# Optimization experiments

Hardware: AMD Instinct MI355X
Metric: run time of the kernel (lower is better)

Reference implementation:

```python
import jax, jax.numpy as jnp
import numpy as np

B, S, D_IN, D_OUT, H = 4, 2048, 1024, 1024, 16
HD = D_OUT // H  # 64


def setup_inputs() -> dict:
    key = jax.random.key(0)
    ks = jax.random.split(key, 6)
    s = 1.0 / np.sqrt(D_IN)
    return {
        "x": jax.random.normal(ks[0], (B, S, D_IN), dtype=jnp.float32),
        "Wq": jax.random.uniform(ks[1], (D_IN, D_OUT), jnp.float32, -s, s),
        "Wk": jax.random.uniform(ks[2], (D_IN, D_OUT), jnp.float32, -s, s),
        "Wv": jax.random.uniform(ks[3], (D_IN, D_OUT), jnp.float32, -s, s),
        "Wo": jax.random.uniform(ks[4], (D_OUT, D_OUT), jnp.float32, -s, s),
        "bo": jax.random.uniform(ks[5], (D_OUT,), jnp.float32, -s, s),
    }


def reference(x, Wq, Wk, Wv, Wo, bo):
    b, s, _ = x.shape
    # QKV projections -> [b, H, s, hd]
    def split_heads(t):
        return t.reshape(b, s, H, HD).transpose(0, 2, 1, 3)
    q = split_heads(x @ Wq)
    k = split_heads(x @ Wk)
    v = split_heads(x @ Wv)
    # attention scores [b, H, s, s]
    scores = jnp.einsum("bhqd,bhkd->bhqk", q, k)
    causal = jnp.triu(jnp.ones((s, s), dtype=bool), k=1)
    scores = jnp.where(causal, -jnp.inf, scores)
    attn = jax.nn.softmax(scores / np.sqrt(HD), axis=-1)
    ctx = jnp.einsum("bhqk,bhkd->bhqd", attn, v)
    ctx = ctx.transpose(0, 2, 1, 3).reshape(b, s, D_OUT)
    return ctx @ Wo + bo
```

## Files before the change

kernel.cpp:

```cpp
#include <hip/hip_runtime.h>

typedef __attribute__((ext_vector_type(8))) short bf16x8;
typedef __attribute__((ext_vector_type(4))) float f32x4;
typedef __attribute__((ext_vector_type(4))) unsigned uint4v;

#define SM_C 0.18033688011112042f
#define MFMA16 __builtin_amdgcn_mfma_f32_16x16x32_bf16

__device__ __forceinline__ unsigned short f2bf(float f) {
  unsigned u = __builtin_bit_cast(unsigned, f);
  u += 0x7fffu + ((u >> 16) & 1u);
  return (unsigned short)(u >> 16);
}

__device__ __forceinline__ unsigned cvtpk(float lo, float hi) {
  unsigned r;
  asm volatile("v_cvt_pk_bf16_f32 %0, %1, %2" : "=v"(r) : "v"(lo), "v"(hi));
  return r;
}

__device__ __forceinline__ void gload16(const void* g, void* lds) {
  __builtin_amdgcn_global_load_lds(
      (const __attribute__((address_space(1))) void*)g,
      (__attribute__((address_space(3))) void*)lds, 16, 0, 0);
}

#define BARRIER __builtin_amdgcn_s_barrier()
#define LGKM0 asm volatile("s_waitcnt lgkmcnt(0)" ::: "memory")

__global__ __launch_bounds__(256) void cvt_x(const float* __restrict__ in,
                                             unsigned short* __restrict__ out,
                                             int n4) {
  int i = blockIdx.x * 256 + threadIdx.x;
  int stride = gridDim.x * 256;
  for (; i < n4; i += stride) {
    float4 v = ((const float4*)in)[i];
    unsigned short o0 = f2bf(v.x), o1 = f2bf(v.y), o2 = f2bf(v.z), o3 = f2bf(v.w);
    unsigned long long packed = (unsigned long long)o0 | ((unsigned long long)o1 << 16) |
                                ((unsigned long long)o2 << 32) | ((unsigned long long)o3 << 48);
    ((unsigned long long*)out)[i] = packed;
  }
}

__global__ __launch_bounds__(256) void transpose_w4(const float* __restrict__ W0,
                                                    const float* __restrict__ W1,
                                                    const float* __restrict__ W2,
                                                    const float* __restrict__ W3,
                                                    unsigned short* __restrict__ WT) {
  __shared__ float tile[32][33];
  const int z = blockIdx.z;
  const float* W = (z == 0) ? W0 : (z == 1) ? W1 : (z == 2) ? W2 : W3;
  unsigned short* WTo = WT + (size_t)z * 1048576;
  int bx = blockIdx.x, by = blockIdx.y;
  int x = bx * 32 + threadIdx.x;
  for (int i = 0; i < 4; ++i) {
    int r = threadIdx.y + i * 8;
    tile[r][threadIdx.x] = W[(by * 32 + r) * 1024 + x];
  }
  __syncthreads();
  int nx = by * 32 + threadIdx.x;
  for (int i = 0; i < 4; ++i) {
    int r = threadIdx.y + i * 8;
    WTo[(long)(bx * 32 + r) * 1024 + nx] = f2bf(tile[threadIdx.x][r]);
  }
}

__global__ __launch_bounds__(256) void transpose_v(const unsigned short* __restrict__ QKV,
                                                   unsigned short* __restrict__ Vt) {
  __shared__ alignas(16) unsigned short tile[64][74];
  const int bid = blockIdx.x;
  const int st = bid & 31, bh = bid >> 5;
  const int b = bh >> 4, h = bh & 15;
  const int t = threadIdx.x;
  const int r = t >> 2, c16 = (t & 3) * 16;
  const unsigned short* src =
      QKV + ((long)(b * 2048 + st * 64 + r)) * 3072 + 2048 + h * 64 + c16;
  uint4v v0 = *(const uint4v*)src;
  uint4v v1 = *(const uint4v*)(src + 8);
  unsigned* dst32 = (unsigned*)&tile[r][c16];
  dst32[0] = v0[0]; dst32[1] = v0[1]; dst32[2] = v0[2]; dst32[3] = v0[3];
  dst32[4] = v1[0]; dst32[5] = v1[1]; dst32[6] = v1[2]; dst32[7] = v1[3];
  __syncthreads();
  const int lw = t & 63, w = t >> 6;
  const int vp = (lw & 32) | (((lw >> 2) & 3) << 3) | (((lw >> 4) & 1) << 2) | (lw & 3);
#pragma unroll
  for (int k = 0; k < 16; ++k) {
    int hd = w * 16 + k;
    Vt[((long)(bh * 64 + hd)) * 2048 + st * 64 + vp] = tile[lw][hd];
  }
}

template <int NR, int FP32OUT>
__global__ __launch_bounds__(512, 1) void gemm2ph(const unsigned short* __restrict__ A,
                                                  const unsigned short* __restrict__ BT,
                                                  unsigned short* __restrict__ Cb,
                                                  float* __restrict__ Cf,
                                                  const float* __restrict__ bias,
                                                  int M, int N, int K) {
  constexpr int BN = NR * 64;
  __shared__ alignas(16) unsigned short As[2][256 * 64];
  __shared__ alignas(16) unsigned short Bs[2][BN * 64];

  const int nbn = N / BN;
  const int tmg = (M / 256) / 8;
  const int cc = blockIdx.x >> 3, xc = blockIdx.x & 7;
  const int tm = xc * tmg + cc / nbn, tn = cc % nbn;

  const int t = threadIdx.x, l = t & 63, wid = t >> 6;
  const int wm = wid >> 2, wn = wid & 3;
  const int lr = l & 15, lg = l >> 4;

  f32x4 acc[8][NR] = {};

  const int sq = t >> 3;
  const int sslot8 = ((t & 7) ^ (sq & 7)) * 8;
  const unsigned short* Ath = A + ((long)tm * 256 + sq) * K + sslot8;
  const unsigned short* Bth = BT + ((long)tn * BN + sq) * K + sslot8;
  const int ldsoff = sq * 64 + (t & 7) * 8;

#define STGA(buf, q, kt) \
  gload16(Ath + (long)((q)*64) * K + (kt)*64, &As[buf][(q)*4096 + ldsoff])
#define STGB(buf, u, kt) \
  gload16(Bth + (long)((u)*64) * K + (kt)*64, &Bs[buf][(u)*4096 + ldsoff])

  const int NT = K >> 6;
#pragma unroll
  for (int u = 0; u < NR; ++u) STGB(0, u, 0);
  STGA(0, 0, 0); STGA(0, 2, 0); STGA(0, 1, 0); STGA(0, 3, 0);

  const int offk0 = (lg ^ (lr & 7)) * 8;
  const int offk1 = ((4 + lg) ^ (lr & 7)) * 8;
  const int arow0 = (wm * 128 + lr) * 64;
  const int brow0 = (wn * (NR * 16) + lr) * 64;

#define DS_A(MH)                                                   \
  _Pragma("unroll") for (int m_ = 0; m_ < 4; ++m_) {               \
    const unsigned short* ap_ = Ac + arow0 + ((MH)*4 + m_) * 1024; \
    af[m_][0] = *(const bf16x8*)(ap_ + offk0);                     \
    af[m_][1] = *(const bf16x8*)(ap_ + offk1);                     \
  }
#define DS_B_ALL                                          \
  _Pragma("unroll") for (int n_ = 0; n_ < NR; ++n_) {     \
    const unsigned short* bp_ = Bc + brow0 + n_ * 1024;   \
    bfr[n_][0] = *(const bf16x8*)(bp_ + offk0);           \
    bfr[n_][1] = *(const bf16x8*)(bp_ + offk1);           \
  }
#define MM(MH)                                                              \
  __builtin_amdgcn_s_setprio(1);                                            \
  _Pragma("unroll") for (int m_ = 0; m_ < 4; ++m_)                          \
  _Pragma("unroll") for (int n_ = 0; n_ < NR; ++n_) {                       \
    acc[(MH)*4 + m_][n_] = MFMA16(af[m_][0], bfr[n_][0],                    \
                                  acc[(MH)*4 + m_][n_], 0, 0, 0);           \
    acc[(MH)*4 + m_][n_] = MFMA16(af[m_][1], bfr[n_][1],                    \
                                  acc[(MH)*4 + m_][n_], 0, 0, 0);           \
  }                                                                         \
  __builtin_amdgcn_s_setprio(0);

  for (int tt = 0; tt < NT; ++tt) {
    const unsigned short* Ac = As[tt & 1];
    const unsigned short* Bc = Bs[tt & 1];
    const int nb = (tt & 1) ^ 1;
    const int kt = tt + 1;
    const bool st = kt < NT;

    bf16x8 af[4][2];
    bf16x8 bfr[NR][2];

    asm volatile("s_waitcnt vmcnt(2)" ::: "memory");
    BARRIER;
    DS_A(0);
    DS_B_ALL;
    if (st) {
#pragma unroll
      for (int u = 0; u < NR; ++u) STGB(nb, u, kt);
    }
    BARRIER;
    LGKM0;
    MM(0);

    if (st) {
      if constexpr (NR == 3) asm volatile("s_waitcnt vmcnt(3)" ::: "memory");
      else                   asm volatile("s_waitcnt vmcnt(2)" ::: "memory");
    } else {
      asm volatile("s_waitcnt vmcnt(0)" ::: "memory");
    }
    BARRIER;
    DS_A(1);
    if (st) { STGA(nb, 0, kt); STGA(nb, 2, kt); STGA(nb, 1, kt); STGA(nb, 3, kt); }
    BARRIER;
    LGKM0;
    MM(1);
  }
#undef DS_A
#undef DS_B_ALL
#undef MM
#undef STGA
#undef STGB

  const long crow = (long)tm * 256 + wm * 128;
  const int ccol = tn * BN + wn * (NR * 16);
#pragma unroll
  for (int m = 0; m < 8; ++m)
#pragma unroll
    for (int n = 0; n < NR; ++n)
#pragma unroll
      for (int r = 0; r < 4; ++r) {
        long row = crow + m * 16 + lg * 4 + r;
        int col = ccol + n * 16 + lr;
        if (FP32OUT)
          Cf[row * N + col] = acc[m][n][r] + bias[col];
        else
          Cb[row * N + col] = f2bf(acc[m][n][r]);
      }
}

template <int TWO>
__device__ __forceinline__ void attn_tile(
    const unsigned short* __restrict__ Kc, const unsigned short* __restrict__ Vc,
    int lr, int lg, bool mask0, bool mask1, int kv0, int q0row, int q1row,
    const bf16x8 (&qf)[2][2], f32x4 (&cacc)[2][4], float (&m_r)[2], float (&l_r)[2]) {
  constexpr int S0 = TWO ? 0 : 1;
  f32x4 p[2][4];
#pragma unroll
  for (int s = S0; s < 2; ++s)
#pragma unroll
    for (int g = 0; g < 4; ++g) p[s][g] = f32x4{0.f, 0.f, 0.f, 0.f};

  __builtin_amdgcn_s_setprio(1);
#pragma unroll
  for (int g = 0; g < 4; ++g) {
    const int key = g * 16 + lr;
    const int swz = (key & 7) << 3;
#pragma unroll
    for (int c = 0; c < 2; ++c) {
      bf16x8 kf = *(const bf16x8*)(Kc + key * 64 + ((c * 32 + lg * 8) ^ swz));
#pragma unroll
      for (int s = S0; s < 2; ++s)
        p[s][g] = MFMA16(kf, qf[s][c], p[s][g], 0, 0, 0);
    }
  }
  __builtin_amdgcn_s_setprio(0);

  if (TWO && mask0) {
#pragma unroll
    for (int g = 0; g < 4; ++g)
#pragma unroll
      for (int r = 0; r < 4; ++r)
        if (kv0 + g * 16 + lg * 4 + r > q0row) p[0][g][r] = -1e30f;
  }
  if (mask1) {
#pragma unroll
    for (int g = 0; g < 4; ++g)
#pragma unroll
      for (int r = 0; r < 4; ++r)
        if (kv0 + g * 16 + lg * 4 + r > q1row) p[1][g][r] = -1e30f;
  }

  unsigned pk[2][4][2];
#pragma unroll
  for (int s = S0; s < 2; ++s) {
    float mloc = p[s][0][0];
#pragma unroll
    for (int g = 0; g < 4; ++g)
#pragma unroll
      for (int r = 0; r < 4; ++r) mloc = fmaxf(mloc, p[s][g][r]);
    mloc = fmaxf(mloc, __shfl_xor(mloc, 16));
    mloc = fmaxf(mloc, __shfl_xor(mloc, 32));
    const bool defer = __all(mloc <= m_r[s] + 44.0f);
    const float mn = defer ? m_r[s] : fmaxf(m_r[s], mloc);
    const float nmc = -mn * SM_C;
    float rs = 0.f;
#pragma unroll
    for (int g = 0; g < 4; ++g)
#pragma unroll
      for (int r = 0; r < 4; ++r) {
        float e = __builtin_amdgcn_exp2f(__builtin_fmaf(p[s][g][r], SM_C, nmc));
        p[s][g][r] = e;
        rs += e;
      }
    rs += __shfl_xor(rs, 16);
    rs += __shfl_xor(rs, 32);
    if (defer) {
      l_r[s] += rs;
    } else {
      float alpha = __builtin_amdgcn_exp2f((m_r[s] - mn) * SM_C);
      l_r[s] = l_r[s] * alpha + rs;
      m_r[s] = mn;
      float alq[4];
#pragma unroll
      for (int r = 0; r < 4; ++r) alq[r] = __shfl(alpha, lg * 20 + r);
#pragma unroll
      for (int n = 0; n < 4; ++n)
#pragma unroll
        for (int r = 0; r < 4; ++r) cacc[s][n][r] *= alq[r];
    }
#pragma unroll
    for (int g = 0; g < 4; ++g) {
      pk[s][g][0] = cvtpk(p[s][g][0], p[s][g][1]);
      pk[s][g][1] = cvtpk(p[s][g][2], p[s][g][3]);
    }
  }

#pragma unroll
  for (int sl = 0; sl < 2; ++sl) {
    bf16x8 vf[4];
#pragma unroll
    for (int n = 0; n < 4; ++n) {
      const int hd = n * 16 + lr;
      vf[n] = *(const bf16x8*)(Vc + hd * 64 + ((sl * 32 + lg * 8) ^ ((hd & 7) << 3)));
    }
    __builtin_amdgcn_s_setprio(1);
#pragma unroll
    for (int s = S0; s < 2; ++s) {
      uint4v pw = {pk[s][2 * sl][0], pk[s][2 * sl][1], pk[s][2 * sl + 1][0], pk[s][2 * sl + 1][1]};
      bf16x8 pa = __builtin_bit_cast(bf16x8, pw);
#pragma unroll
      for (int n = 0; n < 4; ++n)
        cacc[s][n] = MFMA16(pa, vf[n], cacc[s][n], 0, 0, 0);
    }
    __builtin_amdgcn_s_setprio(0);
  }
}

__global__ __launch_bounds__(256, 4) void flash_attn(const unsigned short* __restrict__ QKV,
                                                     const unsigned short* __restrict__ Vt,
                                                     unsigned short* __restrict__ Ctx) {
  __shared__ alignas(16) unsigned short Ks[2][64 * 64];
  __shared__ alignas(16) unsigned short Vs[2][64 * 64];
  const int bid = blockIdx.x;
  const int qt = bid >> 6;
  const int bh = bid & 63;
  const int b = bh >> 4, h = bh & 15;
  const int t = threadIdx.x, l = t & 63, w = t >> 6;
  const int lr = l & 15, lg = l >> 4;
  const long rowbase = (long)b * 2048;
  const int colbase = h * 64;
  const int q0 = qt * 64 + w * 16;
  const int q1 = (31 - qt) * 64 + w * 16;
  const int q0row = q0 + lr, q1row = q1 + lr;
  const int nkv = 32 - qt;

  bf16x8 qf[2][2];
#pragma unroll
  for (int c = 0; c < 2; ++c) {
    qf[0][c] = *(const bf16x8*)(QKV + (rowbase + q0 + lr) * 3072 + colbase + c * 32 + lg * 8);
    qf[1][c] = *(const bf16x8*)(QKV + (rowbase + q1 + lr) * 3072 + colbase + c * 32 + lg * 8);
  }

  f32x4 cacc[2][4];
  float m_r[2], l_r[2];
#pragma unroll
  for (int s = 0; s < 2; ++s) {
    m_r[s] = -1e30f;
    l_r[s] = 0.f;
#pragma unroll
    for (int n = 0; n < 4; ++n) cacc[s][n] = f32x4{0.f, 0.f, 0.f, 0.f};
  }

  const int srow = w * 16 + (l >> 3);
  const int scol = (l & 7) * 8;
  const int kswz = scol ^ ((srow & 7) << 3);
  const unsigned short* kp = QKV + (rowbase + srow) * 3072 + 1024 + colbase + kswz;
  const unsigned short* vp = Vt + ((long)(bh * 64 + srow)) * 2048 + kswz;
  unsigned short* ksd0 = &Ks[0][(w * 16) * 64];
  unsigned short* vsd0 = &Vs[0][(w * 16) * 64];

#define STAGE(buf)                                    \
  do {                                                \
    gload16(kp, ksd0 + (buf) * 4096);                 \
    gload16(kp + 8 * 3072, ksd0 + (buf) * 4096 + 512);\
    gload16(vp, vsd0 + (buf) * 4096);                 \
    gload16(vp + 8 * 2048, vsd0 + (buf) * 4096 + 512);\
    kp += 64 * 3072;                                  \
    vp += 64;                                         \
  } while (0)

  STAGE(0);
  __syncthreads();

  int j = 0;
  for (; j <= qt; ++j) {
    const int cur = j & 1;
    if (j + 1 < nkv) STAGE(cur ^ 1);
    attn_tile<1>(Ks[cur], Vs[cur], lr, lg, j == qt, false, j * 64, q0row, q1row,
                 qf, cacc, m_r, l_r);
    __syncthreads();
  }
  for (; j < nkv; ++j) {
    const int cur = j & 1;
    if (j + 1 < nkv) STAGE(cur ^ 1);
    attn_tile<0>(Ks[cur], Vs[cur], lr, lg, false, j == nkv - 1, j * 64, q0row, q1row,
                 qf, cacc, m_r, l_r);
    __syncthreads();
  }
#undef STAGE

#pragma unroll
  for (int s = 0; s < 2; ++s) {
    float invl = 1.f / l_r[s];
    float ilq[4];
#pragma unroll
    for (int r = 0; r < 4; ++r) ilq[r] = __shfl(invl, lg * 20 + r);
    const int qs = (s == 0) ? q0 : q1;
#pragma unroll
    for (int n = 0; n < 4; ++n)
#pragma unroll
      for (int r = 0; r < 4; ++r) {
        long row = rowbase + qs + lg * 4 + r;
        Ctx[row * 1024 + colbase + n * 16 + lr] = f2bf(cacc[s][n][r] * ilq[r]);
      }
  }
}

extern "C" void kernel_launch(void* const* d_in, const int* in_sizes, int n_in,
                              void* d_out, int out_size, void* d_ws, size_t ws_size,
                              hipStream_t stream) {
  (void)in_sizes; (void)n_in; (void)out_size; (void)ws_size;
  const float* x  = (const float*)d_in[0];
  const float* Wq = (const float*)d_in[1];
  const float* Wk = (const float*)d_in[2];
  const float* Wv = (const float*)d_in[3];
  const float* Wo = (const float*)d_in[4];
  const float* bo = (const float*)d_in[5];
  float* out = (float*)d_out;

  unsigned short* ws = (unsigned short*)d_ws;
  unsigned short* xb  = ws;
  unsigned short* Vt  = ws;
  unsigned short* WqT = ws + 8388608;
  unsigned short* WkT = WqT + 1048576;
  unsigned short* WvT = WkT + 1048576;
  unsigned short* WoT = WvT + 1048576;
  unsigned short* QKV = WoT + 1048576;
  unsigned short* Ctx = QKV + 25165824;

  cvt_x<<<2048, 256, 0, stream>>>(x, xb, 8192 * 1024 / 4);

  dim3 tb(32, 8), tg(32, 32, 4);
  transpose_w4<<<tg, tb, 0, stream>>>(Wq, Wk, Wv, Wo, WqT);

  gemm2ph<3, 0><<<512, 512, 0, stream>>>(xb, WqT, QKV, nullptr, nullptr,
                                         8192, 3072, 1024);

  transpose_v<<<2048, 256, 0, stream>>>(QKV, Vt);

  flash_attn<<<1024, 256, 0, stream>>>(QKV, Vt, Ctx);

  gemm2ph<2, 1><<<256, 512, 0, stream>>>(Ctx, WoT, nullptr, out, bo,
                                         8192, 1024, 1024);
}
```

Before: 160.2 us.

## Triple-buffer A tiles in GEMM to prefetch two K-steps ahead

The GEMM kernel now keeps three LDS buffers for the A operand instead of two. A tiles are prefetched two K-steps ahead while B stays double-buffered. This removes the mid-iteration waitcnt and barrier and gives global loads more time in flight. In exchange LDS use rises to about 144KB per block and the vmcnt bookkeeping becomes more delicate.

```diff
diff --git a/kernel.cpp b/kernel.cpp
--- a/kernel.cpp
+++ b/kernel.cpp
@@ -91,14 +91,14 @@
 }
 
 template <int NR, int FP32OUT>
-__global__ __launch_bounds__(512, 1) void gemm2ph(const unsigned short* __restrict__ A,
-                                                  const unsigned short* __restrict__ BT,
-                                                  unsigned short* __restrict__ Cb,
-                                                  float* __restrict__ Cf,
-                                                  const float* __restrict__ bias,
-                                                  int M, int N, int K) {
+__global__ __launch_bounds__(512, 1) void gemm3b(const unsigned short* __restrict__ A,
+                                                 const unsigned short* __restrict__ BT,
+                                                 unsigned short* __restrict__ Cb,
+                                                 float* __restrict__ Cf,
+                                                 const float* __restrict__ bias,
+                                                 int M, int N, int K) {
   constexpr int BN = NR * 64;
-  __shared__ alignas(16) unsigned short As[2][256 * 64];
+  __shared__ alignas(16) unsigned short As[3][256 * 64];
   __shared__ alignas(16) unsigned short Bs[2][BN * 64];
 
   const int nbn = N / BN;
@@ -125,8 +125,11 @@
 
   const int NT = K >> 6;
 #pragma unroll
+  for (int q = 0; q < 4; ++q) STGA(0, q, 0);
+#pragma unroll
   for (int u = 0; u < NR; ++u) STGB(0, u, 0);
-  STGA(0, 0, 0); STGA(0, 2, 0); STGA(0, 1, 0); STGA(0, 3, 0);
+#pragma unroll
+  for (int q = 0; q < 4; ++q) STGA(1, q, 1);
 
   const int offk0 = (lg ^ (lr & 7)) * 8;
   const int offk1 = ((4 + lg) ^ (lr & 7)) * 8;
@@ -156,40 +159,40 @@
   }                                                                         \
   __builtin_amdgcn_s_setprio(0);
 
+  int cur3 = 0;
+  int stg3 = 2;
   for (int tt = 0; tt < NT; ++tt) {
-    const unsigned short* Ac = As[tt & 1];
+    const unsigned short* Ac = As[cur3];
     const unsigned short* Bc = Bs[tt & 1];
-    const int nb = (tt & 1) ^ 1;
-    const int kt = tt + 1;
-    const bool st = kt < NT;
 
     bf16x8 af[4][2];
     bf16x8 bfr[NR][2];
 
-    asm volatile("s_waitcnt vmcnt(2)" ::: "memory");
+    if (tt == NT - 1) asm volatile("s_waitcnt vmcnt(0)" ::: "memory");
+    else              asm volatile("s_waitcnt vmcnt(4)" ::: "memory");
     BARRIER;
     DS_A(0);
     DS_B_ALL;
-    if (st) {
-#pragma unroll
-      for (int u = 0; u < NR; ++u) STGB(nb, u, kt);
+    if (tt + 1 < NT) {
+      const int nbB = (tt + 1) & 1;
+#pragma unroll
+      for (int u = 0; u < NR; ++u) STGB(nbB, u, tt + 1);
     }
     BARRIER;
     LGKM0;
     MM(0);
 
-    if (st) {
-      if constexpr (NR == 3) asm volatile("s_waitcnt vmcnt(3)" ::: "memory");
-      else                   asm volatile("s_waitcnt vmcnt(2)" ::: "memory");
-    } else {
-      asm volatile("s_waitcnt vmcnt(0)" ::: "memory");
-    }
-    BARRIER;
     DS_A(1);
-    if (st) { STGA(nb, 0, kt); STGA(nb, 2, kt); STGA(nb, 1, kt); STGA(nb, 3, kt); }
+    if (tt + 2 < NT) {
+#pragma unroll
+      for (int q = 0; q < 4; ++q) STGA(stg3, q, tt + 2);
+    }
     BARRIER;
     LGKM0;
     MM(1);
+
+    cur3 = (cur3 == 2) ? 0 : cur3 + 1;
+    stg3 = (stg3 == 2) ? 0 : stg3 + 1;
   }
 #undef DS_A
 #undef DS_B_ALL
@@ -439,13 +442,13 @@
   dim3 tb(32, 8), tg(32, 32, 4);
   transpose_w4<<<tg, tb, 0, stream>>>(Wq, Wk, Wv, Wo, WqT);
 
-  gemm2ph<3, 0><<<512, 512, 0, stream>>>(xb, WqT, QKV, nullptr, nullptr,
-                                         8192, 3072, 1024);
+  gemm3b<3, 0><<<512, 512, 0, stream>>>(xb, WqT, QKV, nullptr, nullptr,
+                                        8192, 3072, 1024);
 
   transpose_v<<<2048, 256, 0, stream>>>(QKV, Vt);
 
   flash_attn<<<1024, 256, 0, stream>>>(QKV, Vt, Ctx);
 
-  gemm2ph<2, 1><<<256, 512, 0, stream>>>(Ctx, WoT, nullptr, out, bo,
-                                         8192, 1024, 1024);
-}
+  gemm3b<2, 1><<<256, 512, 0, stream>>>(Ctx, WoT, nullptr, out, bo,
+                                        8192, 1024, 1024);
+}
```

Measured after the change: 158.2 us. Within noise of the previous version (-1.2%).
